# Optimization experiments

Hardware: AMD Instinct MI355X
Metric: run time of the kernel (lower is better)

## Reference

```python
import jax, jax.numpy as jnp
import numpy as np

B, T, H, N, D, L, V = 4, 1024, 4, 4096, 256, 6, 256
Dh = N // H  # per-head dim; RoPE max_pos == Dh so T <= Dh
EPS = 1e-5


def _ln(x):
    # LayerNorm over last dim, no affine, eps=1e-5 (torch default)
    m = jnp.mean(x, axis=-1, keepdims=True)
    v = jnp.mean((x - m) ** 2, axis=-1, keepdims=True)
    return (x - m) / jnp.sqrt(v + EPS)


def _rope_tables(seq_len, head_dim):
    inv_freq = 1.0 / (10000.0 ** (jnp.arange(0, head_dim, 2, dtype=jnp.float32) / head_dim))
    t = jnp.arange(seq_len, dtype=jnp.float32)
    freqs = jnp.outer(t, inv_freq)            # [T, Dh/2]
    emb = jnp.concatenate([freqs, freqs], -1)  # [T, Dh]
    return jnp.cos(emb), jnp.sin(emb)


def _rotate_half(x):
    d = x.shape[-1]
    return jnp.concatenate([-x[..., d // 2:], x[..., :d // 2]], axis=-1)


def setup_inputs() -> dict:
    key = jax.random.key(0)
    ks = jax.random.split(key, 6)
    tokens = jax.random.randint(ks[0], (B, T), 0, V)
    emb_w = 0.02 * jax.random.normal(ks[1], (V, D), dtype=jnp.float32)
    E = 0.02 * jax.random.normal(ks[2], (N, D), dtype=jnp.float32)
    Dx = 0.02 * jax.random.normal(ks[3], (H, D, Dh), dtype=jnp.float32)
    Dy = 0.02 * jax.random.normal(ks[4], (H, D, Dh), dtype=jnp.float32)
    readout = 0.02 * jax.random.normal(ks[5], (D, V), dtype=jnp.float32)
    return {"tokens": tokens, "emb_w": emb_w, "E": E, "Dx": Dx, "Dy": Dy, "readout": readout}


def reference(tokens, emb_w, E, Dx, Dy, readout):
    b, t = tokens.shape
    dh = Dx.shape[-1]
    cos, sin = _rope_tables(t, dh)  # [T, Dh], broadcast over B,H
    v = _ln(emb_w[tokens])          # [B, T, D]
    for _ in range(L):
        x = jax.nn.relu(jnp.einsum('btd,hde->bhte', v, Dx))       # [B,H,T,Dh]
        xr = x * cos + _rotate_half(x) * sin                       # RoPE (Q and K share)
        scores = jnp.einsum('bhte,bhse->bhts', xr, xr)             # [B,H,T,T] (no softmax)
        a = jnp.einsum('bhts,bsd->bhtd', scores, v)                # [B,H,T,D]
        y = jax.nn.relu(jnp.einsum('bhtd,hde->bhte', a, Dy)) * x   # [B,H,T,Dh]
        y = jnp.transpose(y, (0, 2, 1, 3)).reshape(b, t, -1)       # [B,T,N]
        v = _ln(v + _ln(y @ E))
    return v @ readout  # [B,T,V]
```

## Files before the change

### kernel.cpp

```cpp
#include <hip/hip_runtime.h>
#include <cstdint>

namespace {

typedef _Float16 f16_t;
typedef _Float16 f16x8 __attribute__((ext_vector_type(8)));
typedef _Float16 f16x4 __attribute__((ext_vector_type(4)));
typedef float    f32x4 __attribute__((ext_vector_type(4)));

constexpr int Bc = 4, Tc = 1024, Hc = 4, Dc = 256, DHc = 1024, Lc = 6, Vc = 256;
constexpr int HALFc = 512;
constexpr float EPS = 1e-5f;
constexpr long long T4q  = (long long)Tc * 4096;
constexpr long long TDq  = (long long)Tc * Dc;
constexpr long long DTq  = (long long)Dc * Tc;
constexpr long long HDDq = (long long)DHc * Dc;
constexpr long long TBUFq = (long long)Bc * Tc * Dc;

__device__ __forceinline__ void gload16(const void* g, void* l) {
  __builtin_amdgcn_global_load_lds((const __attribute__((address_space(1))) void*)g,
                                   (__attribute__((address_space(3))) void*)l, 16, 0, 0);
}

template<int EPI, bool BKMAJ, int NW>
__global__ __launch_bounds__(NW * 64)
void gemm_f16(const f16_t* __restrict__ A, long long sAb, long long sAh,
              const f16_t* __restrict__ B, long long sBb, long long sBh,
              void* __restrict__ Cv, long long sCb, long long sCh,
              const f16_t* __restrict__ aux,
              int K, int lda, int ldb, int ldc)
{
  constexpr int FN   = (NW == 4) ? 4 : 2;
  constexpr int NTHR = NW * 64;
  constexpr int SP   = 1024 / NTHR;
  constexpr int RPP  = NTHR / 8;

  __shared__ __align__(16) f16_t As[128 * 64];
  __shared__ __align__(16) f16_t Bs[128 * 64];

  const int zb = blockIdx.z >> 2, zh = blockIdx.z & 3;
  A += zb * sAb + zh * sAh;
  B += zb * sBb + zh * sBh;
  const long long Coff = zb * sCb + zh * sCh;

  const int tid  = threadIdx.x;
  const int lane = tid & 63;
  const int wave = tid >> 6;
  const int wr = (NW == 4) ? (wave >> 1) : (wave >> 2);
  const int wc = (NW == 4) ? (wave & 1)  : (wave & 3);
  const int m0 = blockIdx.y * 128, n0 = blockIdx.x * 128;

  const int lrow  = tid >> 3;
  const int lslot = tid & 7;
  const int kp = tid & 31, g = tid >> 5;

  f32x4 acc[4][FN] = {};

  for (int k0 = 0; k0 < K; k0 += 64) {
    #pragma unroll
    for (int c = 0; c < SP; ++c) {
      const int row  = c * RPP + lrow;
      const int scol = (lslot ^ (row & 7)) << 3;
      gload16(A + (size_t)(m0 + row) * lda + k0 + scol, &As[(c * NTHR + tid) * 8]);
    }
    if (!BKMAJ) {
      #pragma unroll
      for (int c = 0; c < SP; ++c) {
        const int row  = c * RPP + lrow;
        const int scol = (lslot ^ (row & 7)) << 3;
        gload16(B + (size_t)(n0 + row) * ldb + k0 + scol, &Bs[(c * NTHR + tid) * 8]);
      }
    } else {
      constexpr int NP = (NW == 4) ? 2 : 1;
      const int k = kp * 2;
      #pragma unroll
      for (int p = 0; p < NP; ++p) {
        const int nb = p * 64 + g * 8;
        const f16x8 r0 = *(const f16x8*)(B + (size_t)(k0 + k) * ldb + n0 + nb);
        const f16x8 r1 = *(const f16x8*)(B + (size_t)(k0 + k + 1) * ldb + n0 + nb);
        #pragma unroll
        for (int j = 0; j < 8; ++j) {
          const int n = nb + j;
          union { f16_t h[2]; unsigned int u; } pk;
          pk.h[0] = r0[j]; pk.h[1] = r1[j];
          ((unsigned int*)Bs)[n * 32 + (((kp >> 2) ^ (n & 7)) << 2) + (kp & 3)] = pk.u;
        }
      }
    }
    __syncthreads();

    #pragma unroll
    for (int ks = 0; ks < 2; ++ks) {
      f16x8 af[4], bf[FN];
      #pragma unroll
      for (int m = 0; m < 4; ++m) {
        const int r  = wr * 64 + m * 16 + (lane & 15);
        const int sl = (ks * 4 + (lane >> 4)) ^ (r & 7);
        af[m] = *(const f16x8*)(&As[r * 64 + sl * 8]);
      }
      #pragma unroll
      for (int n = 0; n < FN; ++n) {
        const int r  = wc * (FN * 16) + n * 16 + (lane & 15);
        const int sl = (ks * 4 + (lane >> 4)) ^ (r & 7);
        bf[n] = *(const f16x8*)(&Bs[r * 64 + sl * 8]);
      }
      #pragma unroll
      for (int m = 0; m < 4; ++m)
        #pragma unroll
        for (int n = 0; n < FN; ++n)
          acc[m][n] = __builtin_amdgcn_mfma_f32_16x16x32_f16(af[m], bf[n], acc[m][n], 0, 0, 0);
    }
    __syncthreads();
  }

  const int cr   = (lane >> 4) * 4;
  const int ccol = lane & 15;
  if (EPI == 4) {
    float* C = (float*)Cv + Coff;
    #pragma unroll
    for (int m = 0; m < 4; ++m)
      #pragma unroll
      for (int n = 0; n < FN; ++n)
        #pragma unroll
        for (int r = 0; r < 4; ++r)
          C[(long long)(m0 + wr * 64 + m * 16 + cr + r) * ldc
            + (n0 + wc * (FN * 16) + n * 16 + ccol)] = acc[m][n][r];
  } else {
    f16_t* C = (f16_t*)Cv + Coff;
    const f16_t* X = (EPI == 2) ? aux + Coff : nullptr;
    #pragma unroll
    for (int m = 0; m < 4; ++m)
      #pragma unroll
      for (int n = 0; n < FN; ++n)
        #pragma unroll
        for (int r = 0; r < 4; ++r) {
          const long long off = (long long)(m0 + wr * 64 + m * 16 + cr + r) * ldc
                                + (n0 + wc * (FN * 16) + n * 16 + ccol);
          float val = acc[m][n][r];
          if (EPI >= 1) val = fmaxf(val, 0.0f);
          if (EPI == 2) val *= (float)X[off];
          C[off] = (f16_t)val;
        }
  }
}

__global__ __launch_bounds__(256)
void transpose_f32_f16(const float* __restrict__ in, f16_t* __restrict__ out,
                       int R, int C, long long sIn, long long sOut)
{
  __shared__ float tile[32][33];
  in  += (long long)blockIdx.z * sIn;
  out += (long long)blockIdx.z * sOut;
  const int c0 = blockIdx.x * 32, r0 = blockIdx.y * 32;
  const int tx = threadIdx.x & 31, ty = threadIdx.x >> 5;
  #pragma unroll
  for (int i = 0; i < 32; i += 8)
    tile[ty + i][tx] = in[(long long)(r0 + ty + i) * C + (c0 + tx)];
  __syncthreads();
  #pragma unroll
  for (int i = 0; i < 32; i += 8)
    out[(long long)(c0 + ty + i) * R + (r0 + tx)] = (f16_t)tile[tx][ty + i];
}

__global__ __launch_bounds__(256)
void transpose_f16(const f16_t* __restrict__ in, f16_t* __restrict__ out,
                   int R, int C, long long sIn, long long sOut)
{
  __shared__ f16_t tile[32][34];
  in  += (long long)blockIdx.z * sIn;
  out += (long long)blockIdx.z * sOut;
  const int c0 = blockIdx.x * 32, r0 = blockIdx.y * 32;
  const int tx = threadIdx.x & 31, ty = threadIdx.x >> 5;
  #pragma unroll
  for (int i = 0; i < 32; i += 8)
    tile[ty + i][tx] = in[(long long)(r0 + ty + i) * C + (c0 + tx)];
  __syncthreads();
  #pragma unroll
  for (int i = 0; i < 32; i += 8)
    out[(long long)(c0 + ty + i) * R + (r0 + tx)] = tile[tx][ty + i];
}

__global__ __launch_bounds__(256)
void init_tables(float* __restrict__ cosT, float* __restrict__ sinT)
{
  const int i = blockIdx.x * 256 + threadIdx.x;
  const int j = i & (HALFc - 1);
  const int t = i >> 9;
  const float inv = expf(-(float)j * (9.210340371976184f / 512.0f));
  const float ang = (float)t * inv;
  cosT[i] = cosf(ang);
  sinT[i] = sinf(ang);
}

__global__ __launch_bounds__(256)
void rope_f16(const f16_t* __restrict__ x, f16_t* __restrict__ xr,
              const float* __restrict__ cosT, const float* __restrict__ sinT)
{
  const int i   = blockIdx.x * 256 + threadIdx.x;
  const int e4  = i & 127;
  const int bth = i >> 7;
  const int t   = (bth >> 2) & (Tc - 1);
  const f32x4 c = ((const f32x4*)cosT)[t * 128 + e4];
  const f32x4 s = ((const f32x4*)sinT)[t * 128 + e4];
  const long long base = (long long)(bth >> 2) * 4096 + (bth & 3) * DHc + e4 * 4;
  const f16x4 x0 = *(const f16x4*)(x + base);
  const f16x4 x1 = *(const f16x4*)(x + base + HALFc);
  f16x4 r0, r1;
  #pragma unroll
  for (int j = 0; j < 4; ++j) {
    const float a = (float)x0[j], b = (float)x1[j];
    r0[j] = (f16_t)(a * c[j] - b * s[j]);
    r1[j] = (f16_t)(b * c[j] + a * s[j]);
  }
  *(f16x4*)(xr + base) = r0;
  *(f16x4*)(xr + base + HALFc) = r1;
}

__device__ __forceinline__ void block_stats(float val, float* red, float& mean, float& inv_std)
{
  float s1 = val, s2 = val * val;
  #pragma unroll
  for (int o = 1; o < 64; o <<= 1) {
    s1 += __shfl_xor(s1, o);
    s2 += __shfl_xor(s2, o);
  }
  const int lane = threadIdx.x & 63;
  const int w = threadIdx.x >> 6;
  if (lane == 0) { red[w * 2] = s1; red[w * 2 + 1] = s2; }
  __syncthreads();
  s1 = red[0] + red[2] + red[4] + red[6];
  s2 = red[1] + red[3] + red[5] + red[7];
  mean = s1 * (1.0f / Dc);
  const float var = s2 * (1.0f / Dc) - mean * mean;
  inv_std = 1.0f / sqrtf(var + EPS);
  __syncthreads();
}

__global__ __launch_bounds__(256)
void embed_ln(const int* __restrict__ tokens, const float* __restrict__ emb,
              f16_t* __restrict__ v)
{
  __shared__ float red[8];
  const int row = blockIdx.x;
  const int d = threadIdx.x;
  const float val = emb[(long long)tokens[row] * Dc + d];
  float m, is;
  block_stats(val, red, m, is);
  v[(long long)row * Dc + d] = (f16_t)((val - m) * is);
}

__global__ __launch_bounds__(256)
void fuse_ln4(f16_t* __restrict__ v, const float* __restrict__ t)
{
  __shared__ float red[8];
  const long long row = blockIdx.x;
  const int d = threadIdx.x;
  const long long off = row * Dc + d;
  const float tv = t[off] + t[off + TBUFq] + t[off + 2 * TBUFq] + t[off + 3 * TBUFq];
  float m1, is1;
  block_stats(tv, red, m1, is1);
  const float u = (tv - m1) * is1;
  const float wv = (float)v[off] + u;
  float m2, is2;
  block_stats(wv, red, m2, is2);
  v[off] = (f16_t)((wv - m2) * is2);
}

}

extern "C" void kernel_launch(void* const* d_in, const int* in_sizes, int n_in,
                              void* d_out, int out_size, void* d_ws, size_t ws_size,
                              hipStream_t stream)
{
  (void)in_sizes; (void)n_in; (void)out_size; (void)ws_size;
  const int*   tokens  = (const int*)d_in[0];
  const float* emb_w   = (const float*)d_in[1];
  const float* E       = (const float*)d_in[2];
  const float* Dx      = (const float*)d_in[3];
  const float* Dy      = (const float*)d_in[4];
  const float* readout = (const float*)d_in[5];
  float* out = (float*)d_out;

  char* w = (char*)d_ws;
  auto carve = [&](size_t bytes) { char* p = w; w += (bytes + 255) & ~(size_t)255; return p; };
  float* cosT = (float*)carve((size_t)Tc * HALFc * 4);
  float* sinT = (float*)carve((size_t)Tc * HALFc * 4);
  f16_t* v    = (f16_t*)carve((size_t)Bc * Tc * Dc * 2);
  f16_t* vT   = (f16_t*)carve((size_t)Bc * Dc * Tc * 2);
  f16_t* x    = (f16_t*)carve((size_t)Bc * Tc * 4096 * 2);
  f16_t* xr   = (f16_t*)carve((size_t)Bc * Tc * 4096 * 2);
  f16_t* WT   = (f16_t*)carve((size_t)Bc * Dc * 4096 * 2);
  f16_t* a    = (f16_t*)carve((size_t)Bc * Tc * Hc * Dc * 2);
  float* t    = (float*)carve((size_t)4 * TBUFq * 4);
  f16_t* DxT  = (f16_t*)carve((size_t)Hc * DHc * Dc * 2);
  f16_t* DyT  = (f16_t*)carve((size_t)Hc * DHc * Dc * 2);
  f16_t* ET   = (f16_t*)carve((size_t)Dc * Hc * DHc * 2);
  f16_t* RT   = (f16_t*)carve((size_t)Vc * Dc * 2);

  transpose_f32_f16<<<dim3(32, 8, Hc), 256, 0, stream>>>(Dx, DxT, Dc, DHc, HDDq, HDDq);
  transpose_f32_f16<<<dim3(32, 8, Hc), 256, 0, stream>>>(Dy, DyT, Dc, DHc, HDDq, HDDq);
  transpose_f32_f16<<<dim3(8, 128, 1), 256, 0, stream>>>(E, ET, 4096, Dc, 0, 0);
  transpose_f32_f16<<<dim3(8, 8, 1), 256, 0, stream>>>(readout, RT, Dc, Vc, 0, 0);
  init_tables<<<(Tc * HALFc) / 256, 256, 0, stream>>>(cosT, sinT);
  embed_ln<<<Bc * Tc, 256, 0, stream>>>(tokens, emb_w, v);
  transpose_f16<<<dim3(8, 32, Bc), 256, 0, stream>>>(v, vT, Tc, Dc, TDq, DTq);

  for (int l = 0; l < Lc; ++l) {
    gemm_f16<1, false, 4><<<dim3(32, 32, 1), 256, 0, stream>>>(
        v, 0, 0, DxT, 0, 0, x, 0, 0, nullptr, Dc, Dc, Dc, 4096);
    rope_f16<<<(Bc * Tc * Hc * 128) / 256, 256, 0, stream>>>(x, xr, cosT, sinT);
    gemm_f16<0, true, 8><<<dim3(32, 2, 4), 512, 0, stream>>>(
        vT, 0, DTq, xr, 0, T4q, WT, 0, (long long)Dc * 4096, nullptr,
        Tc, Tc, 4096, 4096);
    gemm_f16<0, false, 8><<<dim3(2, 8, 16), 512, 0, stream>>>(
        xr, T4q, DHc, WT, (long long)Dc * 4096, DHc, a, (long long)Tc * 1024, Dc,
        nullptr, DHc, 4096, 4096, 1024);
    gemm_f16<2, false, 4><<<dim3(8, 32, 4), 256, 0, stream>>>(
        a, 0, Dc, DyT, 0, HDDq, xr, 0, DHc, x, Dc, 1024, Dc, 4096);
    gemm_f16<4, false, 8><<<dim3(2, 32, 4), 512, 0, stream>>>(
        xr, 0, DHc, ET, 0, DHc, t, 0, TBUFq, nullptr, DHc, 4096, 4096, Dc);
    fuse_ln4<<<Bc * Tc, 256, 0, stream>>>(v, t);
    transpose_f16<<<dim3(8, 32, Bc), 256, 0, stream>>>(v, vT, Tc, Dc, TDq, DTq);
  }

  gemm_f16<4, false, 8><<<dim3(2, 32, 1), 512, 0, stream>>>(
      v, 0, 0, RT, 0, 0, out, 0, 0, nullptr, Dc, Dc, Dc, Vc);
}
```

Baseline: 823.6 us.

## Fuse RoPE into Dx GEMM epilogue via interleaved head-dim permutation

```diff
diff --git a/kernel.cpp b/kernel.cpp
--- a/kernel.cpp
+++ b/kernel.cpp
@@ -17,6 +17,10 @@
 constexpr long long HDDq = (long long)DHc * Dc;
 constexpr long long TBUFq = (long long)Bc * Tc * Dc;
 
+__device__ __forceinline__ int pe_perm(int v) {
+  return (v & ~1023) | ((v & 511) << 1) | ((v >> 9) & 1);
+}
+
 __device__ __forceinline__ void gload16(const void* g, void* l) {
   __builtin_amdgcn_global_load_lds((const __attribute__((address_space(1))) void*)g,
                                    (__attribute__((address_space(3))) void*)l, 16, 0, 0);
@@ -28,7 +32,8 @@
               const f16_t* __restrict__ B, long long sBb, long long sBh,
               void* __restrict__ Cv, long long sCb, long long sCh,
               const f16_t* __restrict__ aux,
-              int K, int lda, int ldb, int ldc)
+              int K, int lda, int ldb, int ldc,
+              const float* __restrict__ cosP, const float* __restrict__ sinP)
 {
   constexpr int FN   = (NW == 4) ? 4 : 2;
   constexpr int NTHR = NW * 64;
@@ -125,6 +130,30 @@
         for (int r = 0; r < 4; ++r)
           C[(long long)(m0 + wr * 64 + m * 16 + cr + r) * ldc
             + (n0 + wc * (FN * 16) + n * 16 + ccol)] = acc[m][n][r];
+  } else if (EPI == 5) {
+    f16_t* X  = (f16_t*)Cv;
+    f16_t* XR = const_cast<f16_t*>(aux);
+    #pragma unroll
+    for (int m = 0; m < 4; ++m)
+      #pragma unroll
+      for (int n = 0; n < FN; ++n) {
+        const int gcol = n0 + wc * (FN * 16) + n * 16 + ccol;
+        const int jj   = (gcol & 1023) >> 1;
+        const float sg = (gcol & 1) ? 1.0f : -1.0f;
+        #pragma unroll
+        for (int r = 0; r < 4; ++r) {
+          const int grow = m0 + wr * 64 + m * 16 + cr + r;
+          const int tt   = grow & (Tc - 1);
+          const float val  = fmaxf(acc[m][n][r], 0.0f);
+          const float part = __shfl_xor(val, 1);
+          const float c = cosP[tt * HALFc + jj];
+          const float s = sinP[tt * HALFc + jj];
+          const float xrv = val * c + part * s * sg;
+          const long long off = (long long)grow * ldc + gcol;
+          X[off]  = (f16_t)val;
+          XR[off] = (f16_t)xrv;
+        }
+      }
   } else {
     f16_t* C = (f16_t*)Cv + Coff;
     const f16_t* X = (EPI == 2) ? aux + Coff : nullptr;
@@ -146,7 +175,8 @@
 
 __global__ __launch_bounds__(256)
 void transpose_f32_f16(const float* __restrict__ in, f16_t* __restrict__ out,
-                       int R, int C, long long sIn, long long sOut)
+                       int R, int C, long long sIn, long long sOut,
+                       int permR, int permC)
 {
   __shared__ float tile[32][33];
   in  += (long long)blockIdx.z * sIn;
@@ -158,8 +188,13 @@
     tile[ty + i][tx] = in[(long long)(r0 + ty + i) * C + (c0 + tx)];
   __syncthreads();
   #pragma unroll
-  for (int i = 0; i < 32; i += 8)
-    out[(long long)(c0 + ty + i) * R + (r0 + tx)] = (f16_t)tile[tx][ty + i];
+  for (int i = 0; i < 32; i += 8) {
+    int ro = c0 + ty + i;
+    int co = r0 + tx;
+    if (permR) ro = pe_perm(ro);
+    if (permC) co = pe_perm(co);
+    out[(long long)ro * R + co] = (f16_t)tile[tx][ty + i];
+  }
 }
 
 __global__ __launch_bounds__(256)
@@ -190,30 +225,6 @@
   const float ang = (float)t * inv;
   cosT[i] = cosf(ang);
   sinT[i] = sinf(ang);
-}
-
-__global__ __launch_bounds__(256)
-void rope_f16(const f16_t* __restrict__ x, f16_t* __restrict__ xr,
-              const float* __restrict__ cosT, const float* __restrict__ sinT)
-{
-  const int i   = blockIdx.x * 256 + threadIdx.x;
-  const int e4  = i & 127;
-  const int bth = i >> 7;
-  const int t   = (bth >> 2) & (Tc - 1);
-  const f32x4 c = ((const f32x4*)cosT)[t * 128 + e4];
-  const f32x4 s = ((const f32x4*)sinT)[t * 128 + e4];
-  const long long base = (long long)(bth >> 2) * 4096 + (bth & 3) * DHc + e4 * 4;
-  const f16x4 x0 = *(const f16x4*)(x + base);
-  const f16x4 x1 = *(const f16x4*)(x + base + HALFc);
-  f16x4 r0, r1;
-  #pragma unroll
-  for (int j = 0; j < 4; ++j) {
-    const float a = (float)x0[j], b = (float)x1[j];
-    r0[j] = (f16_t)(a * c[j] - b * s[j]);
-    r1[j] = (f16_t)(b * c[j] + a * s[j]);
-  }
-  *(f16x4*)(xr + base) = r0;
-  *(f16x4*)(xr + base + HALFc) = r1;
 }
 
 __device__ __forceinline__ void block_stats(float val, float* red, float& mean, float& inv_std)
@@ -297,32 +308,32 @@
   f16_t* ET   = (f16_t*)carve((size_t)Dc * Hc * DHc * 2);
   f16_t* RT   = (f16_t*)carve((size_t)Vc * Dc * 2);
 
-  transpose_f32_f16<<<dim3(32, 8, Hc), 256, 0, stream>>>(Dx, DxT, Dc, DHc, HDDq, HDDq);
-  transpose_f32_f16<<<dim3(32, 8, Hc), 256, 0, stream>>>(Dy, DyT, Dc, DHc, HDDq, HDDq);
-  transpose_f32_f16<<<dim3(8, 128, 1), 256, 0, stream>>>(E, ET, 4096, Dc, 0, 0);
-  transpose_f32_f16<<<dim3(8, 8, 1), 256, 0, stream>>>(readout, RT, Dc, Vc, 0, 0);
+  transpose_f32_f16<<<dim3(32, 8, Hc), 256, 0, stream>>>(Dx, DxT, Dc, DHc, HDDq, HDDq, 1, 0);
+  transpose_f32_f16<<<dim3(32, 8, Hc), 256, 0, stream>>>(Dy, DyT, Dc, DHc, HDDq, HDDq, 1, 0);
+  transpose_f32_f16<<<dim3(8, 128, 1), 256, 0, stream>>>(E, ET, 4096, Dc, 0, 0, 0, 1);
+  transpose_f32_f16<<<dim3(8, 8, 1), 256, 0, stream>>>(readout, RT, Dc, Vc, 0, 0, 0, 0);
   init_tables<<<(Tc * HALFc) / 256, 256, 0, stream>>>(cosT, sinT);
   embed_ln<<<Bc * Tc, 256, 0, stream>>>(tokens, emb_w, v);
   transpose_f16<<<dim3(8, 32, Bc), 256, 0, stream>>>(v, vT, Tc, Dc, TDq, DTq);
 
   for (int l = 0; l < Lc; ++l) {
-    gemm_f16<1, false, 4><<<dim3(32, 32, 1), 256, 0, stream>>>(
-        v, 0, 0, DxT, 0, 0, x, 0, 0, nullptr, Dc, Dc, Dc, 4096);
-    rope_f16<<<(Bc * Tc * Hc * 128) / 256, 256, 0, stream>>>(x, xr, cosT, sinT);
+    gemm_f16<5, false, 4><<<dim3(32, 32, 1), 256, 0, stream>>>(
+        v, 0, 0, DxT, 0, 0, x, 0, 0, xr, Dc, Dc, Dc, 4096, cosT, sinT);
     gemm_f16<0, true, 8><<<dim3(32, 2, 4), 512, 0, stream>>>(
         vT, 0, DTq, xr, 0, T4q, WT, 0, (long long)Dc * 4096, nullptr,
-        Tc, Tc, 4096, 4096);
+        Tc, Tc, 4096, 4096, nullptr, nullptr);
     gemm_f16<0, false, 8><<<dim3(2, 8, 16), 512, 0, stream>>>(
         xr, T4q, DHc, WT, (long long)Dc * 4096, DHc, a, (long long)Tc * 1024, Dc,
-        nullptr, DHc, 4096, 4096, 1024);
+        nullptr, DHc, 4096, 4096, 1024, nullptr, nullptr);
     gemm_f16<2, false, 4><<<dim3(8, 32, 4), 256, 0, stream>>>(
-        a, 0, Dc, DyT, 0, HDDq, xr, 0, DHc, x, Dc, 1024, Dc, 4096);
+        a, 0, Dc, DyT, 0, HDDq, xr, 0, DHc, x, Dc, 1024, Dc, 4096, nullptr, nullptr);
     gemm_f16<4, false, 8><<<dim3(2, 32, 4), 512, 0, stream>>>(
-        xr, 0, DHc, ET, 0, DHc, t, 0, TBUFq, nullptr, DHc, 4096, 4096, Dc);
+        xr, 0, DHc, ET, 0, DHc, t, 0, TBUFq, nullptr, DHc, 4096, 4096, Dc,
+        nullptr, nullptr);
     fuse_ln4<<<Bc * Tc, 256, 0, stream>>>(v, t);
     transpose_f16<<<dim3(8, 32, Bc), 256, 0, stream>>>(v, vT, Tc, Dc, TDq, DTq);
   }
 
   gemm_f16<4, false, 8><<<dim3(2, 32, 1), 512, 0, stream>>>(
-      v, 0, 0, RT, 0, 0, out, 0, 0, nullptr, Dc, Dc, Dc, Vc);
-}
+      v, 0, 0, RT, 0, 0, out, 0, 0, nullptr, Dc, Dc, Dc, Vc, nullptr, nullptr);
+}
```

Result: no change. 810.6 us (-1.6%).
